# Kernel tuning notes

Hardware: AMD Instinct MI355X
Metric: run time of the kernel (lower is better)

The kernel has to match this reference:

```python
import jax, jax.numpy as jnp
from jax import lax
import numpy as np

B = 64          # batch
HW = 28         # image height/width (hardcoded in module)
LATENT = 256    # latent_size
LABEL = 10      # label_size
FEAT = 64 * HW * HW  # 50176, encoder/decoder fc feature dim


def _conv(x, w, pad):
    # x: [N,C,H,W], w: [O,I,kH,kW]
    return lax.conv_general_dilated(
        x, w, (1, 1), ((pad, pad), (pad, pad)),
        dimension_numbers=('NCHW', 'OIHW', 'NCHW'))


def _conv_transpose(x, w, b, pad):
    # ConvTranspose2d(stride=1, padding=pad) == conv with flipped, transposed
    # kernel and padding k-1-pad. w: [I,O,kH,kW] (torch ConvTranspose layout).
    k = w.shape[2]
    wt = jnp.flip(w, (2, 3)).transpose(1, 0, 2, 3)  # [O,I,kH,kW]
    return _conv(x, wt, k - 1 - pad) + b[None, :, None, None]


def _encoder(images, c1w, c1b, c2w, c2b, fcw, fcb):
    x = jax.nn.relu(_conv(images, c1w, 2) + c1b[None, :, None, None])
    x = jax.nn.relu(_conv(x, c2w, 2) + c2b[None, :, None, None])
    x = x.reshape(x.shape[0], FEAT)
    return jnp.tanh(x @ fcw.T + fcb)


def _decoder(z, fcw, fcb, ct2w, ct2b, ct1w, ct1b):
    x = jnp.arctanh(z)
    x = (x @ fcw.T + fcb).reshape(-1, 64, HW, HW)
    x = jax.nn.relu(_conv_transpose(x, ct2w, ct2b, 2))
    return _conv_transpose(x, ct1w, ct1b, 2)


def _hopfield_weight(patterns):
    # TrainHopfield: Hebbian outer-product sum with mean subtraction,
    # zero diagonal, normalized by number of patterns. One GEMM.
    rho = jnp.mean(patterns)
    t = patterns - rho                      # [L, latent]
    w = t.T @ t                             # [latent, latent]
    w = w - jnp.diag(jnp.diag(w))
    return w / patterns.shape[0]


def _cluster(s0, w):
    # Batched version of: iterate s = sign(w @ s) up to LATENT steps,
    # stopping per-sample when energy -s@w@s stops changing.
    def energy(s):
        return -jnp.einsum('bi,ij,bj->b', s, w, s)

    def step(carry, _):
        s, prev_e, done = carry
        new_s = jnp.sign(s @ w.T)           # w symmetric; per-sample w@s
        e = energy(new_s)
        s_next = jnp.where(done[:, None], s, new_s)
        prev_e_next = jnp.where(done, prev_e, e)
        done_next = done | (e == prev_e)
        return (s_next, prev_e_next, done_next), None

    init = (s0, energy(s0), jnp.zeros(s0.shape[0], dtype=bool))
    (s, _, _), _ = lax.scan(step, init, None, length=LATENT)
    return s


def setup_inputs() -> dict:
    key = jax.random.key(0)
    ks = jax.random.split(key, 12)
    s = 0.05
    f32 = jnp.float32
    return {
        'images': jax.random.normal(ks[0], (B, 1, HW, HW), f32),
        'enc_c1_w': jax.random.normal(ks[1], (32, 1, 5, 5), f32) * s,
        'enc_c1_b': jnp.zeros((32,), f32),
        'enc_c2_w': jax.random.normal(ks[2], (64, 32, 5, 5), f32) * s,
        'enc_c2_b': jnp.zeros((64,), f32),
        'enc_fc_w': jax.random.normal(ks[3], (LATENT, FEAT), f32) * 0.005,
        'enc_fc_b': jnp.zeros((LATENT,), f32),
        'dec_fc_w': jax.random.normal(ks[4], (FEAT, LATENT), f32) * s,
        'dec_fc_b': jnp.zeros((FEAT,), f32),
        'dec_ct2_w': jax.random.normal(ks[5], (64, 32, 5, 5), f32) * s,
        'dec_ct2_b': jnp.zeros((32,), f32),
        'dec_ct1_w': jax.random.normal(ks[6], (32, 1, 5, 5), f32) * s,
        'dec_ct1_b': jnp.zeros((1,), f32),
        'sm_w': jax.random.normal(ks[7], (LABEL, LATENT), f32) * s,
        'sm_b': jnp.zeros((LABEL,), f32),
        'label_latent': jnp.tanh(jax.random.normal(ks[8], (LABEL, LATENT), f32)),
    }


def reference(images, enc_c1_w, enc_c1_b, enc_c2_w, enc_c2_b, enc_fc_w,
              enc_fc_b, dec_fc_w, dec_fc_b, dec_ct2_w, dec_ct2_b, dec_ct1_w,
              dec_ct1_b, sm_w, sm_b, label_latent):
    z = _encoder(images, enc_c1_w, enc_c1_b, enc_c2_w, enc_c2_b,
                 enc_fc_w, enc_fc_b)                       # [B, latent]
    w = _hopfield_weight(jnp.sign(label_latent))           # [latent, latent]
    s0 = lax.stop_gradient(jnp.sign(z))                    # detached copy
    clustered = _cluster(s0, w)                            # [B, latent]
    cluster_probs = jax.nn.softmax(clustered @ label_latent.T, axis=1)
    class_probs = jax.nn.softmax(z @ sm_w.T + sm_b, axis=1)
    recon = _decoder(z, dec_fc_w, dec_fc_b, dec_ct2_w, dec_ct2_b,
                     dec_ct1_w, dec_ct1_b)                 # [B,1,28,28]
    return (cluster_probs, class_probs, recon)
```

## Files before the change

### kernel.cpp

```cpp
#include <hip/hip_runtime.h>
#include <hip/hip_bf16.h>
#include <math.h>

#define BATCH 64
#define HW 28
#define PIX 784
#define LATENT 256
#define LABEL 10
#define FEAT 50176
#define KS 98
#define TSTR 36

typedef __attribute__((ext_vector_type(8))) short bf16x8;
typedef __attribute__((ext_vector_type(4))) float f32x4;

__device__ __forceinline__ float sgnf(float v) {
    return (v > 0.f) ? 1.f : ((v < 0.f) ? -1.f : 0.f);
}

__device__ __forceinline__ short f2bf(float f) {
    union { float f; unsigned u; } v; v.f = f;
    unsigned r = v.u + 0x7FFF + ((v.u >> 16) & 1);
    return (short)(r >> 16);
}
__device__ __forceinline__ float bf2f(short s) {
    union { unsigned u; float f; } v; v.u = ((unsigned)(unsigned short)s) << 16;
    return v.f;
}

__device__ __forceinline__ void split3(const float* __restrict__ p,
                                       bf16x8& h, bf16x8& m, bf16x8& l) {
    float4 a = *(const float4*)p;
    float4 b = *(const float4*)(p + 4);
    float v[8] = {a.x, a.y, a.z, a.w, b.x, b.y, b.z, b.w};
    #pragma unroll
    for (int j = 0; j < 8; ++j) {
        short s0 = f2bf(v[j]); float r = v[j] - bf2f(s0);
        short s1 = f2bf(r);    float r2 = r - bf2f(s1);
        h[j] = s0; m[j] = s1; l[j] = f2bf(r2);
    }
}

template<int G, int FLIP>
__global__ __launch_bounds__(256) void conv5_k(const float* __restrict__ in,
                        const float* __restrict__ w,
                        const float* __restrict__ bias, float* __restrict__ out,
                        int IC, int OC, int relu) {
    int b = blockIdx.x, oc0 = blockIdx.y * G;
    __shared__ float plp[2][32 * TSTR];
    int tid = threadIdx.x;

    for (int t = tid; t < 2 * 32 * TSTR; t += 256) ((float*)plp)[t] = 0.f;

    bool actS = tid < 196;
    int ys = tid / 7, qs = tid % 7;

    int q = tid & 7, yy = tid >> 3;
    bool actC = (q < 7) && (yy < 28);
    int x0 = q * 4;

    float acc[G][4];
    #pragma unroll
    for (int g = 0; g < G; ++g)
        #pragma unroll
        for (int xi = 0; xi < 4; ++xi) acc[g][xi] = 0.f;

    __syncthreads();
    if (actS) {
        float4 v = *(const float4*)&in[((size_t)(b * IC + 0)) * PIX + tid * 4];
        *(float2*)&plp[0][(ys + 2) * TSTR + 4 * qs + 2] = make_float2(v.x, v.y);
        *(float2*)&plp[0][(ys + 2) * TSTR + 4 * qs + 4] = make_float2(v.z, v.w);
    }
    __syncthreads();

    for (int ic = 0; ic < IC; ++ic) {
        float4 vn;
        bool more = (ic + 1) < IC;
        if (more && actS)
            vn = *(const float4*)&in[((size_t)(b * IC + ic + 1)) * PIX + tid * 4];

        const float* tile = plp[ic & 1];
        if (actC) {
            #pragma unroll
            for (int dy = 0; dy < 5; ++dy) {
                float4 ra = *(const float4*)&tile[(yy + dy) * TSTR + x0];
                float4 rb = *(const float4*)&tile[(yy + dy) * TSTR + x0 + 4];
                float rw[8] = {ra.x, ra.y, ra.z, ra.w, rb.x, rb.y, rb.z, rb.w};
                #pragma unroll
                for (int g = 0; g < G; ++g) {
                    #pragma unroll
                    for (int dx = 0; dx < 5; ++dx) {
                        float wv = FLIP
                            ? w[((size_t)ic * OC + (oc0 + g)) * 25 + (4 - dy) * 5 + (4 - dx)]
                            : w[((size_t)(oc0 + g) * IC + ic) * 25 + dy * 5 + dx];
                        #pragma unroll
                        for (int xi = 0; xi < 4; ++xi)
                            acc[g][xi] += rw[xi + dx] * wv;
                    }
                }
            }
        }
        if (more && actS) {
            float* nt = plp[(ic + 1) & 1];
            *(float2*)&nt[(ys + 2) * TSTR + 4 * qs + 2] = make_float2(vn.x, vn.y);
            *(float2*)&nt[(ys + 2) * TSTR + 4 * qs + 4] = make_float2(vn.z, vn.w);
        }
        __syncthreads();
    }

    if (actC) {
        #pragma unroll
        for (int g = 0; g < G; ++g) {
            float bv = bias[oc0 + g];
            float4 o;
            o.x = acc[g][0] + bv;
            o.y = acc[g][1] + bv;
            o.z = acc[g][2] + bv;
            o.w = acc[g][3] + bv;
            if (relu) {
                o.x = fmaxf(o.x, 0.f); o.y = fmaxf(o.y, 0.f);
                o.z = fmaxf(o.z, 0.f); o.w = fmaxf(o.w, 0.f);
            }
            *(float4*)&out[((size_t)(b * OC + (oc0 + g))) * PIX + yy * HW + x0] = o;
        }
    }
}

__global__ __launch_bounds__(256) void c2_mfma_k(const short* __restrict__ xh,
                        const short* __restrict__ xm, const short* __restrict__ xl,
                        const short* __restrict__ wb,
                        const float* __restrict__ bias, float* __restrict__ out) {
    int b = blockIdx.x;
    int t0 = blockIdx.y * 4;
    int tid = threadIdx.x;
    int wv = tid >> 6;
    int lane = tid & 63;
    int prow = lane & 15, kgrp = lane >> 4;

    f32x4 acc[4][4];
    #pragma unroll
    for (int pt = 0; pt < 4; ++pt)
        #pragma unroll
        for (int nt = 0; nt < 4; ++nt) acc[pt][nt] = (f32x4){0.f, 0.f, 0.f, 0.f};

    int py[4], px[4];
    bool ptv[4];
    #pragma unroll
    for (int pt = 0; pt < 4; ++pt) {
        int p = (t0 + pt) * 16 + prow;
        ptv[pt] = (t0 + pt) < 49;
        py[pt] = p / 28; px[pt] = p % 28;
    }

    for (int tap = wv; tap < 25; tap += 4) {
        int dy = tap / 5 - 2, dx = tap % 5 - 2;
        const short* wt = wb + (size_t)tap * 2048;
        bf16x8 B0[4], B1[4], B2[4];
        #pragma unroll
        for (int nt = 0; nt < 4; ++nt) {
            int off = (nt * 16 + prow) * 32 + kgrp * 8;
            B0[nt] = *(const bf16x8*)&wt[off];
            B1[nt] = *(const bf16x8*)&wt[51200 + off];
            B2[nt] = *(const bf16x8*)&wt[102400 + off];
        }
        #pragma unroll
        for (int pt = 0; pt < 4; ++pt) {
            int ysrc = py[pt] + dy, xsrc = px[pt] + dx;
            bool valid = ptv[pt] && (ysrc >= 0) && (ysrc < 28) && (xsrc >= 0) && (xsrc < 28);
            bf16x8 ah = {0,0,0,0,0,0,0,0}, am = {0,0,0,0,0,0,0,0}, al = {0,0,0,0,0,0,0,0};
            if (valid) {
                size_t o = ((size_t)b * PIX + ysrc * 28 + xsrc) * 32 + kgrp * 8;
                ah = *(const bf16x8*)&xh[o];
                am = *(const bf16x8*)&xm[o];
                al = *(const bf16x8*)&xl[o];
            }
            #pragma unroll
            for (int nt = 0; nt < 4; ++nt) {
                acc[pt][nt] = __builtin_amdgcn_mfma_f32_16x16x32_bf16(ah, B0[nt], acc[pt][nt], 0, 0, 0);
                acc[pt][nt] = __builtin_amdgcn_mfma_f32_16x16x32_bf16(ah, B1[nt], acc[pt][nt], 0, 0, 0);
                acc[pt][nt] = __builtin_amdgcn_mfma_f32_16x16x32_bf16(am, B0[nt], acc[pt][nt], 0, 0, 0);
                acc[pt][nt] = __builtin_amdgcn_mfma_f32_16x16x32_bf16(ah, B2[nt], acc[pt][nt], 0, 0, 0);
                acc[pt][nt] = __builtin_amdgcn_mfma_f32_16x16x32_bf16(am, B1[nt], acc[pt][nt], 0, 0, 0);
                acc[pt][nt] = __builtin_amdgcn_mfma_f32_16x16x32_bf16(al, B0[nt], acc[pt][nt], 0, 0, 0);
            }
        }
    }

    __shared__ float red[3][64][64];
    if (wv > 0) {
        #pragma unroll
        for (int pt = 0; pt < 4; ++pt)
            #pragma unroll
            for (int nt = 0; nt < 4; ++nt)
                #pragma unroll
                for (int r = 0; r < 4; ++r)
                    red[wv - 1][lane][pt * 16 + nt * 4 + r] = acc[pt][nt][r];
    }
    __syncthreads();
    if (wv == 0) {
        #pragma unroll
        for (int pt = 0; pt < 4; ++pt)
            #pragma unroll
            for (int nt = 0; nt < 4; ++nt)
                #pragma unroll
                for (int r = 0; r < 4; ++r) {
                    int ix = pt * 16 + nt * 4 + r;
                    float s = acc[pt][nt][r];
                    s += red[0][lane][ix];
                    s += red[1][lane][ix];
                    s += red[2][lane][ix];
                    acc[pt][nt][r] = s;
                }

        __shared__ float ot[64][17];
        float bv = bias[lane];
        for (int pt = 0; pt < 4; ++pt) {
            if (!ptv[pt]) continue;
            #pragma unroll
            for (int nt = 0; nt < 4; ++nt)
                #pragma unroll
                for (int r = 0; r < 4; ++r)
                    ot[nt * 16 + prow][kgrp * 4 + r] = acc[pt][nt][r];
            float* op = &out[((size_t)(b * 64 + lane)) * PIX + (t0 + pt) * 16];
            #pragma unroll
            for (int i = 0; i < 4; ++i) {
                float4 o;
                o.x = fmaxf(ot[lane][i * 4 + 0] + bv, 0.f);
                o.y = fmaxf(ot[lane][i * 4 + 1] + bv, 0.f);
                o.z = fmaxf(ot[lane][i * 4 + 2] + bv, 0.f);
                o.w = fmaxf(ot[lane][i * 4 + 3] + bv, 0.f);
                *(float4*)&op[i * 4] = o;
            }
        }
    }
}

__global__ void xsplit3_k(const float* __restrict__ x, short* __restrict__ xh,
                          short* __restrict__ xm, short* __restrict__ xl) {
    __shared__ float lds[32][17];
    int b = blockIdx.x, pbase = blockIdx.y * 16;
    int t = threadIdx.x;
    if (t < 128) {
        int ic = t >> 2, pj = (t & 3) * 4;
        float4 v = *(const float4*)&x[((size_t)(b * 32 + ic)) * PIX + pbase + pj];
        lds[ic][pj + 0] = v.x; lds[ic][pj + 1] = v.y;
        lds[ic][pj + 2] = v.z; lds[ic][pj + 3] = v.w;
    }
    __syncthreads();
    int p = t >> 4, ic2 = (t & 15) * 2;
    size_t o = ((size_t)b * PIX + pbase + p) * 32 + ic2;
    short2 h, m, l;
    {
        float v = lds[ic2][p];
        short s0 = f2bf(v); float r = v - bf2f(s0);
        short s1 = f2bf(r); float r2 = r - bf2f(s1);
        h.x = s0; m.x = s1; l.x = f2bf(r2);
    }
    {
        float v = lds[ic2 + 1][p];
        short s0 = f2bf(v); float r = v - bf2f(s0);
        short s1 = f2bf(r); float r2 = r - bf2f(s1);
        h.y = s0; m.y = s1; l.y = f2bf(r2);
    }
    *(short2*)&xh[o] = h;
    *(short2*)&xm[o] = m;
    *(short2*)&xl[o] = l;
}

__global__ void wprep3_k(const float* __restrict__ w, short* __restrict__ wb) {
    int j = blockIdx.x * 256 + threadIdx.x;
    if (j < 51200) {
        int ic = j & 31;
        int oc = (j >> 5) & 63;
        int tap = j >> 11;
        float v = w[((size_t)oc * 32 + ic) * 25 + tap];
        short s0 = f2bf(v); float r = v - bf2f(s0);
        short s1 = f2bf(r); float r2 = r - bf2f(s1);
        wb[j] = s0;
        wb[51200 + j] = s1;
        wb[102400 + j] = f2bf(r2);
    }
}

__global__ __launch_bounds__(64) void ct2_mfma_k(const short* __restrict__ xb,
                        const short* __restrict__ wb,
                        const float* __restrict__ bias, float* __restrict__ out) {
    int b = blockIdx.x;
    int pbase = blockIdx.y * 16;
    int lane = threadIdx.x;
    int prow = lane & 15;
    int kgrp = lane >> 4;
    int p = pbase + prow;
    int py = p / 28, px = p % 28;

    f32x4 acc0 = {0.f, 0.f, 0.f, 0.f};
    f32x4 acc1 = {0.f, 0.f, 0.f, 0.f};

    for (int tap = 0; tap < 25; ++tap) {
        int dy = tap / 5 - 2, dx = tap % 5 - 2;
        int ysrc = py + dy, xsrc = px + dx;
        bool valid = (ysrc >= 0) && (ysrc < 28) && (xsrc >= 0) && (xsrc < 28);
        int ps = ysrc * 28 + xsrc;

        bf16x8 a0 = {0,0,0,0,0,0,0,0}, a1 = {0,0,0,0,0,0,0,0};
        if (valid) {
            const bf16x8* ap = (const bf16x8*)&xb[((size_t)b * PIX + ps) * 64 + kgrp * 8];
            a0 = ap[0];
            a1 = ap[4];
        }
        const short* wt = &wb[(size_t)tap * 32 * 64];
        int oc_l = lane & 15;
        bf16x8 b00 = *(const bf16x8*)&wt[oc_l * 64 + kgrp * 8];
        bf16x8 b01 = *(const bf16x8*)&wt[oc_l * 64 + 32 + kgrp * 8];
        bf16x8 b10 = *(const bf16x8*)&wt[(16 + oc_l) * 64 + kgrp * 8];
        bf16x8 b11 = *(const bf16x8*)&wt[(16 + oc_l) * 64 + 32 + kgrp * 8];

        acc0 = __builtin_amdgcn_mfma_f32_16x16x32_bf16(a0, b00, acc0, 0, 0, 0);
        acc0 = __builtin_amdgcn_mfma_f32_16x16x32_bf16(a1, b01, acc0, 0, 0, 0);
        acc1 = __builtin_amdgcn_mfma_f32_16x16x32_bf16(a0, b10, acc1, 0, 0, 0);
        acc1 = __builtin_amdgcn_mfma_f32_16x16x32_bf16(a1, b11, acc1, 0, 0, 0);
    }

    __shared__ float ot[32][16];
    int drow = (lane >> 4) * 4;
    #pragma unroll
    for (int r = 0; r < 4; ++r) {
        ot[lane & 15][drow + r]        = acc0[r];
        ot[16 + (lane & 15)][drow + r] = acc1[r];
    }
    __syncthreads();
    int oc = lane >> 1, ph = (lane & 1) * 8;
    float bv = bias[oc];
    float4 o0, o1;
    o0.x = fmaxf(ot[oc][ph + 0] + bv, 0.f);
    o0.y = fmaxf(ot[oc][ph + 1] + bv, 0.f);
    o0.z = fmaxf(ot[oc][ph + 2] + bv, 0.f);
    o0.w = fmaxf(ot[oc][ph + 3] + bv, 0.f);
    o1.x = fmaxf(ot[oc][ph + 4] + bv, 0.f);
    o1.y = fmaxf(ot[oc][ph + 5] + bv, 0.f);
    o1.z = fmaxf(ot[oc][ph + 6] + bv, 0.f);
    o1.w = fmaxf(ot[oc][ph + 7] + bv, 0.f);
    float* op = &out[((size_t)(b * 32 + oc)) * PIX + pbase + ph];
    *(float4*)&op[0] = o0;
    *(float4*)&op[4] = o1;
}

__global__ void wprep_k(const float* __restrict__ w, short* __restrict__ wb) {
    int j = blockIdx.x * 256 + threadIdx.x;
    if (j < 25 * 32 * 64) {
        int ic = j & 63;
        int oc = (j >> 6) & 31;
        int tap = j >> 11;
        int dyi = tap / 5, dxi = tap % 5;
        wb[j] = f2bf(w[((size_t)ic * 32 + oc) * 25 + (4 - dyi) * 5 + (4 - dxi)]);
    }
}

__global__ void xpose16_k(const short* __restrict__ y16, short* __restrict__ xb) {
    __shared__ short lds[64][16];
    int b = blockIdx.x, pbase = blockIdx.y * 16;
    int t = threadIdx.x;
    {
        int ic = t >> 2, pj = (t & 3) * 4;
        short4 v = *(const short4*)&y16[((size_t)(b * 64 + ic)) * PIX + pbase + pj];
        lds[ic][pj + 0] = v.x;
        lds[ic][pj + 1] = v.y;
        lds[ic][pj + 2] = v.z;
        lds[ic][pj + 3] = v.w;
    }
    __syncthreads();
    {
        int p = t >> 4, icq = (t & 15) * 4;
        short4 s;
        s.x = lds[icq + 0][p];
        s.y = lds[icq + 1][p];
        s.z = lds[icq + 2][p];
        s.w = lds[icq + 3][p];
        *(short4*)&xb[((size_t)b * PIX + pbase + p) * 64 + icq] = s;
    }
}

__global__ __launch_bounds__(512) void enc_fc_mfma_k(const float* __restrict__ x,
                        const float* __restrict__ w, float* __restrict__ part) {
    int ks = blockIdx.x;
    int nh = blockIdx.y;
    int kbase = ks * 512;
    int tid = threadIdx.x;
    int lane = tid & 63, wv = tid >> 6;
    int prow = lane & 15, kgrp = lane >> 4;
    int nrow = nh * 128 + wv * 16 + prow;

    f32x4 acc[4];
    #pragma unroll
    for (int mt = 0; mt < 4; ++mt) acc[mt] = (f32x4){0.f, 0.f, 0.f, 0.f};

    for (int kt = 0; kt < 16; ++kt) {
        int kof = kbase + kt * 32 + kgrp * 8;
        bf16x8 bh, bm, bl;
        split3(&w[(size_t)nrow * FEAT + kof], bh, bm, bl);
        #pragma unroll
        for (int mt = 0; mt < 4; ++mt) {
            bf16x8 ah, am, al;
            split3(&x[(size_t)(mt * 16 + prow) * FEAT + kof], ah, am, al);
            acc[mt] = __builtin_amdgcn_mfma_f32_16x16x32_bf16(ah, bh, acc[mt], 0, 0, 0);
            acc[mt] = __builtin_amdgcn_mfma_f32_16x16x32_bf16(ah, bm, acc[mt], 0, 0, 0);
            acc[mt] = __builtin_amdgcn_mfma_f32_16x16x32_bf16(am, bh, acc[mt], 0, 0, 0);
            acc[mt] = __builtin_amdgcn_mfma_f32_16x16x32_bf16(ah, bl, acc[mt], 0, 0, 0);
            acc[mt] = __builtin_amdgcn_mfma_f32_16x16x32_bf16(am, bm, acc[mt], 0, 0, 0);
            acc[mt] = __builtin_amdgcn_mfma_f32_16x16x32_bf16(al, bh, acc[mt], 0, 0, 0);
        }
    }

    __shared__ float ot[64 * 129];
    #pragma unroll
    for (int mt = 0; mt < 4; ++mt)
        #pragma unroll
        for (int r = 0; r < 4; ++r) {
            int m = mt * 16 + kgrp * 4 + r;
            ot[m * 129 + wv * 16 + prow] = acc[mt][r];
        }
    __syncthreads();
    int m = tid >> 3, c0 = (tid & 7) * 4;
    float* pp = &part[(size_t)ks * BATCH * LATENT + m * 256 + nh * 128];
    #pragma unroll
    for (int i = 0; i < 4; ++i) {
        int n = c0 + i * 32;
        *(float4*)&pp[n] = *(float4*)&ot[m * 129 + n];
    }
}

__global__ void enc_fc_fin_k(const float* __restrict__ part, const float* __restrict__ bias,
                             float* __restrict__ z, short* __restrict__ xah,
                             short* __restrict__ xam) {
    int m = blockIdx.x;
    int n = threadIdx.x;
    int idx = m * 256 + n;
    float a = bias[n];
    for (int ksi = 0; ksi < KS; ++ksi) a += part[(size_t)ksi * BATCH * LATENT + idx];
    float zv = tanhf(a);
    z[idx] = zv;
    float xv = atanhf(zv);
    short h = f2bf(xv);
    xah[idx] = h;
    xam[idx] = f2bf(xv - bf2f(h));
}

__global__ void hop_rho_k(const float* __restrict__ ll, float* __restrict__ rho_out) {
    float p = 0.f;
    for (int t = threadIdx.x; t < LABEL * LATENT; t += 256) p += sgnf(ll[t]);
    __shared__ float red[8];
    for (int o = 32; o; o >>= 1) p += __shfl_down(p, o, 64);
    if ((threadIdx.x & 63) == 0) red[threadIdx.x >> 6] = p;
    __syncthreads();
    if (threadIdx.x == 0)
        rho_out[0] = (red[0] + red[1] + red[2] + red[3]) / (float)(LABEL * LATENT);
}

__global__ void hop_w_k(const float* __restrict__ ll, const float* __restrict__ rho_p,
                        float* __restrict__ wout) {
    int i = blockIdx.x, j = threadIdx.x;
    float rho = rho_p[0];
    float acc = 0.f;
    #pragma unroll
    for (int l = 0; l < LABEL; ++l) {
        float a = sgnf(ll[l * LATENT + i]) - rho;
        float b = sgnf(ll[l * LATENT + j]) - rho;
        acc += a * b;
    }
    wout[i * LATENT + j] = (i == j) ? 0.f : acc / 10.f;
}

__global__ __launch_bounds__(1024) void cluster_k(const float* __restrict__ z,
                          const float* __restrict__ w,
                          const float* __restrict__ ll, float* __restrict__ out) {
    int b = blockIdx.x;
    int t = threadIdx.x;
    int i = t & 255;
    int q = t >> 8;
    int lane = t & 63;
    int wvid = t >> 6;

    __shared__ float s_sh[LATENT];
    __shared__ float part[1024];
    __shared__ float red[4];
    __shared__ float cflag[4];
    __shared__ int ctl_sh;
    __shared__ float logit[LABEL];

    float wreg[64];
    #pragma unroll
    for (int jj = 0; jj < 64; ++jj)
        wreg[jj] = w[(q * 64 + jj) * LATENT + i];

    float s_cur = 0.f, s_old = 2.f, v = 0.f;
    float e_prev = 0.f;
    if (q == 0) {
        s_cur = sgnf(z[b * LATENT + i]);
        s_sh[i] = s_cur;
    }
    __syncthreads();

    {
        float p0 = 0.f, p1 = 0.f;
        #pragma unroll
        for (int jj = 0; jj < 64; jj += 2) {
            p0 += wreg[jj]     * s_sh[q * 64 + jj];
            p1 += wreg[jj + 1] * s_sh[q * 64 + jj + 1];
        }
        part[t] = p0 + p1;
    }
    __syncthreads();
    if (q == 0) {
        v = part[i] + part[i + 256] + part[i + 512] + part[i + 768];
        float p = s_cur * v;
        #pragma unroll
        for (int o = 32; o; o >>= 1) p += __shfl_down(p, o, 64);
        if (lane == 0) red[wvid] = p;
    }
    __syncthreads();
    if (t == 0) e_prev = -(red[0] + red[1] + red[2] + red[3]);

    for (int it = 0; it < LATENT; ++it) {
        if (q == 0) {
            float ns = sgnf(v);
            unsigned long long m = __ballot(ns == s_old);
            if (lane == 0) cflag[wvid] = (m == ~0ull) ? 1.f : 0.f;
            s_sh[i] = ns;
            s_old = s_cur;
            s_cur = ns;
        }
        __syncthreads();
        {
            float p0 = 0.f, p1 = 0.f;
            #pragma unroll
            for (int jj = 0; jj < 64; jj += 2) {
                p0 += wreg[jj]     * s_sh[q * 64 + jj];
                p1 += wreg[jj + 1] * s_sh[q * 64 + jj + 1];
            }
            part[t] = p0 + p1;
        }
        __syncthreads();
        if (q == 0) {
            v = part[i] + part[i + 256] + part[i + 512] + part[i + 768];
            float p = s_cur * v;
            #pragma unroll
            for (int o = 32; o; o >>= 1) p += __shfl_down(p, o, 64);
            if (lane == 0) red[wvid] = p;
        }
        __syncthreads();
        if (t == 0) {
            float e = -(red[0] + red[1] + red[2] + red[3]);
            int c = 0;
            if (e == e_prev) c = 1;
            else if (it >= 1 && cflag[0] != 0.f && cflag[1] != 0.f &&
                     cflag[2] != 0.f && cflag[3] != 0.f)
                c = (((LATENT - 1 - it) & 1) == 0) ? 2 : 3;
            else e_prev = e;
            ctl_sh = c;
        }
        __syncthreads();
        int c = ctl_sh;
        if (c != 0) {
            if (c == 3 && q == 0) s_sh[i] = s_old;
            break;
        }
    }
    __syncthreads();

    if (wvid < LABEL) {
        float p = 0.f;
        #pragma unroll
        for (int r = 0; r < 4; ++r)
            p += s_sh[r * 64 + lane] * ll[wvid * LATENT + r * 64 + lane];
        #pragma unroll
        for (int o = 32; o; o >>= 1) p += __shfl_down(p, o, 64);
        if (lane == 0) logit[wvid] = p;
    }
    __syncthreads();
    if (t == 0) {
        float mx = logit[0];
        for (int c = 1; c < LABEL; ++c) mx = fmaxf(mx, logit[c]);
        float ex[LABEL];
        float s = 0.f;
        for (int c = 0; c < LABEL; ++c) { ex[c] = expf(logit[c] - mx); s += ex[c]; }
        for (int c = 0; c < LABEL; ++c) out[b * LABEL + c] = ex[c] / s;
    }
}

__device__ __forceinline__ float block_sum256(float p, float* red) {
    __syncthreads();
    for (int o = 32; o; o >>= 1) p += __shfl_down(p, o, 64);
    if ((threadIdx.x & 63) == 0) red[threadIdx.x >> 6] = p;
    __syncthreads();
    return red[0] + red[1] + red[2] + red[3];
}

__global__ void class_k(const float* __restrict__ z, const float* __restrict__ smw,
                        const float* __restrict__ smb, float* __restrict__ out) {
    int b = blockIdx.x;
    int i = threadIdx.x;
    __shared__ float red[8];
    __shared__ float logit[LABEL];
    float zi = z[b * LATENT + i];
    for (int c = 0; c < LABEL; ++c) {
        float p = zi * smw[c * LATENT + i];
        float t = block_sum256(p, red);
        if (i == 0) logit[c] = t + smb[c];
    }
    __syncthreads();
    if (i == 0) {
        float mx = logit[0];
        for (int c = 1; c < LABEL; ++c) mx = fmaxf(mx, logit[c]);
        float ex[LABEL];
        float s = 0.f;
        for (int c = 0; c < LABEL; ++c) { ex[c] = expf(logit[c] - mx); s += ex[c]; }
        for (int c = 0; c < LABEL; ++c) out[b * LABEL + c] = ex[c] / s;
    }
}

__global__ __launch_bounds__(256) void dec_fc_mfma_k(const short* __restrict__ xah,
                         const short* __restrict__ xam,
                         const float* __restrict__ w,
                         const float* __restrict__ bias, short* __restrict__ y16) {
    int tid = threadIdx.x;
    int lane = tid & 63, wv = tid >> 6;
    int prow = lane & 15, kgrp = lane >> 4;
    int n0 = blockIdx.x * 64;
    int nb = n0 + wv * 16;

    f32x4 acc[4];
    #pragma unroll
    for (int mi = 0; mi < 4; ++mi) acc[mi] = (f32x4){0.f, 0.f, 0.f, 0.f};

    for (int kc = 0; kc < 8; ++kc) {
        int kof = kc * 32 + kgrp * 8;
        const float* wp = &w[(size_t)(nb + prow) * LATENT + kof];
        float4 w0 = *(const float4*)&wp[0];
        float4 w1 = *(const float4*)&wp[4];
        bf16x8 bf;
        bf[0] = f2bf(w0.x); bf[1] = f2bf(w0.y); bf[2] = f2bf(w0.z); bf[3] = f2bf(w0.w);
        bf[4] = f2bf(w1.x); bf[5] = f2bf(w1.y); bf[6] = f2bf(w1.z); bf[7] = f2bf(w1.w);
        #pragma unroll
        for (int mi = 0; mi < 4; ++mi) {
            bf16x8 ah = *(const bf16x8*)&xah[(mi * 16 + prow) * LATENT + kof];
            bf16x8 am = *(const bf16x8*)&xam[(mi * 16 + prow) * LATENT + kof];
            acc[mi] = __builtin_amdgcn_mfma_f32_16x16x32_bf16(ah, bf, acc[mi], 0, 0, 0);
            acc[mi] = __builtin_amdgcn_mfma_f32_16x16x32_bf16(am, bf, acc[mi], 0, 0, 0);
        }
    }

    __shared__ short ot[64 * 72];
    float bv = bias[nb + prow];
    #pragma unroll
    for (int mi = 0; mi < 4; ++mi)
        #pragma unroll
        for (int r = 0; r < 4; ++r) {
            int m = mi * 16 + kgrp * 4 + r;
            ot[m * 72 + wv * 16 + prow] = f2bf(acc[mi][r] + bv);
        }
    __syncthreads();
    int m = tid >> 2, q = tid & 3;
    #pragma unroll
    for (int i = 0; i < 2; ++i) {
        *(int4*)&y16[(size_t)m * FEAT + n0 + i * 32 + q * 8] =
            *(int4*)&ot[m * 72 + i * 32 + q * 8];
    }
}

extern "C" void kernel_launch(void* const* d_in, const int* in_sizes, int n_in,
                              void* d_out, int out_size, void* d_ws, size_t ws_size,
                              hipStream_t stream) {
    const float* images   = (const float*)d_in[0];
    const float* c1w      = (const float*)d_in[1];
    const float* c1b      = (const float*)d_in[2];
    const float* c2w      = (const float*)d_in[3];
    const float* c2b      = (const float*)d_in[4];
    const float* efw      = (const float*)d_in[5];
    const float* efb      = (const float*)d_in[6];
    const float* dfw      = (const float*)d_in[7];
    const float* dfb      = (const float*)d_in[8];
    const float* ct2w     = (const float*)d_in[9];
    const float* ct2b     = (const float*)d_in[10];
    const float* ct1w     = (const float*)d_in[11];
    const float* ct1b     = (const float*)d_in[12];
    const float* smw      = (const float*)d_in[13];
    const float* smb      = (const float*)d_in[14];
    const float* ll       = (const float*)d_in[15];

    float* out = (float*)d_out;
    float* ws  = (float*)d_ws;

    float* big0 = ws;
    float* big1 = ws + 3211264;
    float* z    = ws + 3211264 + 1605632 + 458752;
    float* whop = z + BATCH * LATENT;
    float* rho  = whop + LATENT * LATENT;
    float* xsa  = rho + 4;
    short* xah  = (short*)xsa;
    short* xam  = xah + 16384;
    short* xbf  = (short*)(xsa + 16384);
    short* wbf  = (short*)(xsa + 16384 + 1605632);
    short* xh3  = xbf;
    short* xm3  = xbf + 1605632;
    short* xl3  = (short*)(xsa + 16384 + 1605632 + 25600);
    short* wb3  = xl3 + 1605632;
    short* y16  = (short*)big0;
    float* part = (float*)xbf;

    conv5_k<4,0><<<dim3(BATCH, 8), 256, 0, stream>>>(images, c1w, c1b, big1, 1, 32, 1);
    wprep3_k<<<200, 256, 0, stream>>>(c2w, wb3);
    xsplit3_k<<<dim3(BATCH, 49), 256, 0, stream>>>(big1, xh3, xm3, xl3);
    c2_mfma_k<<<dim3(BATCH, 13), 256, 0, stream>>>(xh3, xm3, xl3, wb3, c2b, big0);
    enc_fc_mfma_k<<<dim3(KS, 2), 512, 0, stream>>>(big0, efw, part);
    enc_fc_fin_k<<<BATCH, 256, 0, stream>>>(part, efb, z, xah, xam);

    hop_rho_k<<<1, 256, 0, stream>>>(ll, rho);
    hop_w_k<<<LATENT, 256, 0, stream>>>(ll, rho, whop);
    cluster_k<<<BATCH, 1024, 0, stream>>>(z, whop, ll, out);
    class_k<<<BATCH, 256, 0, stream>>>(z, smw, smb, out + 640);

    wprep_k<<<200, 256, 0, stream>>>(ct2w, wbf);
    dec_fc_mfma_k<<<FEAT / 64, 256, 0, stream>>>(xah, xam, dfw, dfb, y16);
    xpose16_k<<<dim3(BATCH, 49), 256, 0, stream>>>(y16, xbf);
    ct2_mfma_k<<<dim3(BATCH, 49), 64, 0, stream>>>(xbf, wbf, ct2b, big1);
    conv5_k<1,1><<<dim3(BATCH, 1), 256, 0, stream>>>(big1, ct1w, ct1b, out + 1280, 32, 1, 0);
}
```

Before: 305.4 us.

## Use single-wave conv2 blocks and double the encoder FC split-K factor

The conv2 MFMA kernel now runs one wavefront per block and loops over all 25 taps, which removes the cross-wave LDS reduction and the barrier. Its input loads are made unconditional by clamping the address and zeroing afterward. The encoder FC split-K count goes from 98 to 196 slices, with partial sums spread over two scratch buffers, to give the large weight stream more parallelism. In exchange, conv2 has four times fewer waves doing serial work per block, and the final reduction reads twice as many partials.

```diff
diff --git a/kernel.cpp b/kernel.cpp
--- a/kernel.cpp
+++ b/kernel.cpp
@@ -8,7 +8,7 @@
 #define LATENT 256
 #define LABEL 10
 #define FEAT 50176
-#define KS 98
+#define KS 196
 #define TSTR 36
 
 typedef __attribute__((ext_vector_type(8))) short bf16x8;
@@ -126,15 +126,13 @@
     }
 }
 
-__global__ __launch_bounds__(256) void c2_mfma_k(const short* __restrict__ xh,
+__global__ __launch_bounds__(64) void c2_mfma_k(const short* __restrict__ xh,
                         const short* __restrict__ xm, const short* __restrict__ xl,
                         const short* __restrict__ wb,
                         const float* __restrict__ bias, float* __restrict__ out) {
     int b = blockIdx.x;
     int t0 = blockIdx.y * 4;
-    int tid = threadIdx.x;
-    int wv = tid >> 6;
-    int lane = tid & 63;
+    int lane = threadIdx.x;
     int prow = lane & 15, kgrp = lane >> 4;
 
     f32x4 acc[4][4];
@@ -152,7 +150,8 @@
         py[pt] = p / 28; px[pt] = p % 28;
     }
 
-    for (int tap = wv; tap < 25; tap += 4) {
+    const bf16x8 zero8 = {0,0,0,0,0,0,0,0};
+    for (int tap = 0; tap < 25; ++tap) {
         int dy = tap / 5 - 2, dx = tap % 5 - 2;
         const short* wt = wb + (size_t)tap * 2048;
         bf16x8 B0[4], B1[4], B2[4];
@@ -167,13 +166,12 @@
         for (int pt = 0; pt < 4; ++pt) {
             int ysrc = py[pt] + dy, xsrc = px[pt] + dx;
             bool valid = ptv[pt] && (ysrc >= 0) && (ysrc < 28) && (xsrc >= 0) && (xsrc < 28);
-            bf16x8 ah = {0,0,0,0,0,0,0,0}, am = {0,0,0,0,0,0,0,0}, al = {0,0,0,0,0,0,0,0};
-            if (valid) {
-                size_t o = ((size_t)b * PIX + ysrc * 28 + xsrc) * 32 + kgrp * 8;
-                ah = *(const bf16x8*)&xh[o];
-                am = *(const bf16x8*)&xm[o];
-                al = *(const bf16x8*)&xl[o];
-            }
+            int yc = min(max(ysrc, 0), 27), xc = min(max(xsrc, 0), 27);
+            size_t o = ((size_t)b * PIX + yc * 28 + xc) * 32 + kgrp * 8;
+            bf16x8 ah = *(const bf16x8*)&xh[o];
+            bf16x8 am = *(const bf16x8*)&xm[o];
+            bf16x8 al = *(const bf16x8*)&xl[o];
+            if (!valid) { ah = zero8; am = zero8; al = zero8; }
             #pragma unroll
             for (int nt = 0; nt < 4; ++nt) {
                 acc[pt][nt] = __builtin_amdgcn_mfma_f32_16x16x32_bf16(ah, B0[nt], acc[pt][nt], 0, 0, 0);
@@ -186,51 +184,24 @@
         }
     }
 
-    __shared__ float red[3][64][64];
-    if (wv > 0) {
-        #pragma unroll
-        for (int pt = 0; pt < 4; ++pt)
+    __shared__ float ot[64][17];
+    float bv = bias[lane];
+    for (int pt = 0; pt < 4; ++pt) {
+        if (!ptv[pt]) continue;
+        #pragma unroll
+        for (int nt = 0; nt < 4; ++nt)
             #pragma unroll
-            for (int nt = 0; nt < 4; ++nt)
-                #pragma unroll
-                for (int r = 0; r < 4; ++r)
-                    red[wv - 1][lane][pt * 16 + nt * 4 + r] = acc[pt][nt][r];
-    }
-    __syncthreads();
-    if (wv == 0) {
-        #pragma unroll
-        for (int pt = 0; pt < 4; ++pt)
-            #pragma unroll
-            for (int nt = 0; nt < 4; ++nt)
-                #pragma unroll
-                for (int r = 0; r < 4; ++r) {
-                    int ix = pt * 16 + nt * 4 + r;
-                    float s = acc[pt][nt][r];
-                    s += red[0][lane][ix];
-                    s += red[1][lane][ix];
-                    s += red[2][lane][ix];
-                    acc[pt][nt][r] = s;
-                }
-
-        __shared__ float ot[64][17];
-        float bv = bias[lane];
-        for (int pt = 0; pt < 4; ++pt) {
-            if (!ptv[pt]) continue;
-            #pragma unroll
-            for (int nt = 0; nt < 4; ++nt)
-                #pragma unroll
-                for (int r = 0; r < 4; ++r)
-                    ot[nt * 16 + prow][kgrp * 4 + r] = acc[pt][nt][r];
-            float* op = &out[((size_t)(b * 64 + lane)) * PIX + (t0 + pt) * 16];
-            #pragma unroll
-            for (int i = 0; i < 4; ++i) {
-                float4 o;
-                o.x = fmaxf(ot[lane][i * 4 + 0] + bv, 0.f);
-                o.y = fmaxf(ot[lane][i * 4 + 1] + bv, 0.f);
-                o.z = fmaxf(ot[lane][i * 4 + 2] + bv, 0.f);
-                o.w = fmaxf(ot[lane][i * 4 + 3] + bv, 0.f);
-                *(float4*)&op[i * 4] = o;
-            }
+            for (int r = 0; r < 4; ++r)
+                ot[nt * 16 + prow][kgrp * 4 + r] = acc[pt][nt][r];
+        float* op = &out[((size_t)(b * 64 + lane)) * PIX + (t0 + pt) * 16];
+        #pragma unroll
+        for (int i = 0; i < 4; ++i) {
+            float4 o;
+            o.x = fmaxf(ot[lane][i * 4 + 0] + bv, 0.f);
+            o.y = fmaxf(ot[lane][i * 4 + 1] + bv, 0.f);
+            o.z = fmaxf(ot[lane][i * 4 + 2] + bv, 0.f);
+            o.w = fmaxf(ot[lane][i * 4 + 3] + bv, 0.f);
+            *(float4*)&op[i * 4] = o;
         }
     }
 }
@@ -381,10 +352,11 @@
 }
 
 __global__ __launch_bounds__(512) void enc_fc_mfma_k(const float* __restrict__ x,
-                        const float* __restrict__ w, float* __restrict__ part) {
+                        const float* __restrict__ w,
+                        float* __restrict__ pA, float* __restrict__ pB) {
     int ks = blockIdx.x;
     int nh = blockIdx.y;
-    int kbase = ks * 512;
+    int kbase = ks * 256;
     int tid = threadIdx.x;
     int lane = tid & 63, wv = tid >> 6;
     int prow = lane & 15, kgrp = lane >> 4;
@@ -394,7 +366,7 @@
     #pragma unroll
     for (int mt = 0; mt < 4; ++mt) acc[mt] = (f32x4){0.f, 0.f, 0.f, 0.f};
 
-    for (int kt = 0; kt < 16; ++kt) {
+    for (int kt = 0; kt < 8; ++kt) {
         int kof = kbase + kt * 32 + kgrp * 8;
         bf16x8 bh, bm, bl;
         split3(&w[(size_t)nrow * FEAT + kof], bh, bm, bl);
@@ -420,8 +392,10 @@
             ot[m * 129 + wv * 16 + prow] = acc[mt][r];
         }
     __syncthreads();
+    float* base = (ks < 98) ? (pA + (size_t)ks * BATCH * LATENT)
+                            : (pB + (size_t)(ks - 98) * BATCH * LATENT);
     int m = tid >> 3, c0 = (tid & 7) * 4;
-    float* pp = &part[(size_t)ks * BATCH * LATENT + m * 256 + nh * 128];
+    float* pp = &base[m * 256 + nh * 128];
     #pragma unroll
     for (int i = 0; i < 4; ++i) {
         int n = c0 + i * 32;
@@ -429,14 +403,16 @@
     }
 }
 
-__global__ void enc_fc_fin_k(const float* __restrict__ part, const float* __restrict__ bias,
+__global__ void enc_fc_fin_k(const float* __restrict__ pA, const float* __restrict__ pB,
+                             const float* __restrict__ bias,
                              float* __restrict__ z, short* __restrict__ xah,
                              short* __restrict__ xam) {
     int m = blockIdx.x;
     int n = threadIdx.x;
     int idx = m * 256 + n;
     float a = bias[n];
-    for (int ksi = 0; ksi < KS; ++ksi) a += part[(size_t)ksi * BATCH * LATENT + idx];
+    for (int ksi = 0; ksi < 98; ++ksi) a += pA[(size_t)ksi * BATCH * LATENT + idx];
+    for (int ksi = 0; ksi < 98; ++ksi) a += pB[(size_t)ksi * BATCH * LATENT + idx];
     float zv = tanhf(a);
     z[idx] = zv;
     float xv = atanhf(zv);
@@ -705,14 +681,15 @@
     short* xl3  = (short*)(xsa + 16384 + 1605632 + 25600);
     short* wb3  = xl3 + 1605632;
     short* y16  = (short*)big0;
-    float* part = (float*)xbf;
+    float* partA = big1;
+    float* partB = (float*)xbf;
 
     conv5_k<4,0><<<dim3(BATCH, 8), 256, 0, stream>>>(images, c1w, c1b, big1, 1, 32, 1);
     wprep3_k<<<200, 256, 0, stream>>>(c2w, wb3);
     xsplit3_k<<<dim3(BATCH, 49), 256, 0, stream>>>(big1, xh3, xm3, xl3);
-    c2_mfma_k<<<dim3(BATCH, 13), 256, 0, stream>>>(xh3, xm3, xl3, wb3, c2b, big0);
-    enc_fc_mfma_k<<<dim3(KS, 2), 512, 0, stream>>>(big0, efw, part);
-    enc_fc_fin_k<<<BATCH, 256, 0, stream>>>(part, efb, z, xah, xam);
+    c2_mfma_k<<<dim3(BATCH, 13), 64, 0, stream>>>(xh3, xm3, xl3, wb3, c2b, big0);
+    enc_fc_mfma_k<<<dim3(KS, 2), 512, 0, stream>>>(big0, efw, partA, partB);
+    enc_fc_fin_k<<<BATCH, 256, 0, stream>>>(partA, partB, efb, z, xah, xam);
 
     hop_rho_k<<<1, 256, 0, stream>>>(ll, rho);
     hop_w_k<<<LATENT, 256, 0, stream>>>(ll, rho, whop);
```

Result: no change. 304.8 us (-0.2%).
